# Performance work log

Hardware: AMD Instinct MI355X
Metric: run time of the kernel (lower is better)

The kernel has to match this reference:

```python
import jax, jax.numpy as jnp
import numpy as np

N = 100000   # nodes
E = 1000000  # edges (before self-loops)
IN = 128     # in_channel
HID = 32     # hidden_channels
H1 = 8       # in_head
OUT = 40     # out_channel
NEG_SLOPE = 0.2


def setup_inputs() -> dict:
    key = jax.random.key(0)
    ks = jax.random.split(key, 12)
    s = 0.05
    return {
        "x0": jax.random.normal(ks[0], (N, IN), jnp.float32),
        "W1": jax.random.normal(ks[1], (IN, H1 * HID), jnp.float32) * s,
        "att_src1": jax.random.normal(ks[2], (H1, HID), jnp.float32) * s,
        "att_dst1": jax.random.normal(ks[3], (H1, HID), jnp.float32) * s,
        "b1": jnp.zeros((H1 * HID,), jnp.float32),
        "W2": jax.random.normal(ks[4], (H1 * HID, 1 * HID), jnp.float32) * s,
        "att_src2": jax.random.normal(ks[5], (1, HID), jnp.float32) * s,
        "att_dst2": jax.random.normal(ks[6], (1, HID), jnp.float32) * s,
        "b2": jnp.zeros((HID,), jnp.float32),
        "linW": jax.random.normal(ks[7], (HID, OUT), jnp.float32) * s,
        "linb": jnp.zeros((OUT,), jnp.float32),
        "edge_index": jax.random.randint(ks[8], (2, E), 0, N, dtype=jnp.int64),
    }


def gat_conv(x, src, dst, W, att_src, att_dst, bias, concat):
    # PyG GATConv (eval mode): per-head linear, edge attention, dst-softmax, scatter-add
    H, C = att_src.shape
    h = (x @ W).reshape(N, H, C)                       # [N,H,C]
    a_src = jnp.sum(h * att_src[None], axis=-1)        # [N,H]
    a_dst = jnp.sum(h * att_dst[None], axis=-1)        # [N,H]
    alpha = jax.nn.leaky_relu(a_src[src] + a_dst[dst], NEG_SLOPE)  # [Etot,H]
    m = jax.ops.segment_max(alpha, dst, num_segments=N)           # [N,H]
    ea = jnp.exp(alpha - m[dst])
    denom = jax.ops.segment_sum(ea, dst, num_segments=N)
    w = ea / jnp.clip(denom, 1e-16, None)[dst]          # [Etot,H]
    out = jax.ops.segment_sum(w[:, :, None] * h[src], dst, num_segments=N)  # [N,H,C]
    out = out.reshape(N, H * C) if concat else jnp.mean(out, axis=1)
    return out + bias


def reference(x0, W1, att_src1, att_dst1, b1, W2, att_src2, att_dst2, b2, linW, linb, edge_index):
    # add self-loops (PyG add_self_loops=True default)
    loop = jnp.arange(N, dtype=edge_index.dtype)
    src = jnp.concatenate([edge_index[0], loop])
    dst = jnp.concatenate([edge_index[1], loop])
    # dropout layers are no-ops in eval mode
    x1 = gat_conv(x0, src, dst, W1, att_src1, att_dst1, b1, concat=True)   # [N, 8*HID]
    x2 = jax.nn.relu(x1)
    x2 = gat_conv(x2, src, dst, W2, att_src2, att_dst2, b2, concat=False)  # [N, HID]
    return x2 @ linW + linb                                                 # [N, OUT]
```

## Files before the change

### kernel.cpp

```cpp
#include <hip/hip_runtime.h>

#define N 100000
#define E 1000000
#define ETOT 1100000
#define NB1 391
#define NBE 4297
#define NBH (NBE * 8)
#define NBG 782
#define BUCKET 12500

typedef __attribute__((ext_vector_type(8))) short bf16x8;
typedef __attribute__((ext_vector_type(4))) float f32x4;
typedef __attribute__((ext_vector_type(2))) float f32x2;

__device__ __forceinline__ float lrelu(float x) { return x > 0.f ? x : 0.2f * x; }
__device__ __forceinline__ unsigned short f2b(float x) {
    unsigned u = __float_as_uint(x);
    return (unsigned short)((u + 0x7FFFu + ((u >> 16) & 1u)) >> 16);
}
__device__ __forceinline__ float b2f(unsigned short v) {
    return __uint_as_float(((unsigned)v) << 16);
}
__device__ __forceinline__ unsigned char f2q(float x) {
    return (unsigned char)(__builtin_amdgcn_cvt_pk_fp8_f32(x, x, 0, false) & 0xFF);
}

__global__ __launch_bounds__(256) void prep_kernel(const int* __restrict__ ei,
                                                   int* __restrict__ hist,
                                                   const float* __restrict__ W1,
                                                   const float* __restrict__ W2,
                                                   const float* __restrict__ att_src1,
                                                   const float* __restrict__ att_dst1,
                                                   unsigned short* __restrict__ W1T,
                                                   unsigned short* __restrict__ W2T) {
    const int b = blockIdx.x;
    const int t = threadIdx.x;
    if (b < NBH) {
        const int w = b >> 3;
        const int k = b & 7;
        const int e = w * 256 + t;
        if (e < ETOT) {
            int d = (e < E) ? ei[E + e] : (e - E);
            if (d / BUCKET == k) atomicAdd(&hist[d], 1);
        }
        return;
    }
    const int bb = b - NBH;
    if (bb < 128) {
        W1T[(size_t)t * 128 + bb] = f2b(W1[(size_t)bb * 256 + t]);
    } else if (bb < 160) {
        int n = bb - 128;
        W2T[(size_t)n * 256 + t] = f2b(W2[(size_t)t * 32 + n]);
    } else {
        int idx = (bb - 160) * 256 + t;
        int col = idx >> 7;
        int k = idx & 127;
        int h = col & 7;
        const float* att = (col < 8) ? att_src1 : att_dst1;
        float acc = 0.f;
#pragma unroll 8
        for (int j = 0; j < 32; j++) acc += W1[(size_t)k * 256 + h * 32 + j] * att[h * 32 + j];
        W1T[(size_t)(256 + col) * 128 + k] = f2b(acc);
    }
}

__global__ __launch_bounds__(256) void g1s_kernel(const float* __restrict__ x0,
                                                  const unsigned short* __restrict__ W1T,
                                                  unsigned char* __restrict__ h1,
                                                  float* __restrict__ a_src,
                                                  float* __restrict__ a_dst,
                                                  const int* __restrict__ hist,
                                                  int* __restrict__ rofs,
                                                  int* __restrict__ bsum) {
    __shared__ int sm[256];
    if (blockIdx.x >= NBG) {
        const int blk = blockIdx.x - NBG;
        const int t = threadIdx.x;
        const int i = blk * 256 + t;
        int v = (i < N) ? hist[i] : 0;
        sm[t] = v;
        __syncthreads();
#pragma unroll
        for (int off = 1; off < 256; off <<= 1) {
            int x = (t >= off) ? sm[t - off] : 0;
            __syncthreads();
            sm[t] += x;
            __syncthreads();
        }
        if (i < N) rofs[i] = sm[t] - v;
        if (t == 255) bsum[blk] = sm[255];
        return;
    }
    const int wv = threadIdx.x >> 6;
    const int lane = threadIdx.x & 63;
    const int quad = lane >> 4, c = lane & 15;
    const int base_m = blockIdx.x * 128 + wv * 32;
    const int l = c & 3;
    const unsigned sel1 = (l & 1) ? 0x07030501u : 0x02060004u;
    const unsigned sel2 = (l & 2) ? 0x07060302u : 0x01000504u;
    bf16x8 af[2][4];
#pragma unroll
    for (int mt = 0; mt < 2; mt++) {
        int row = base_m + mt * 16 + c;
        int rowc = row < N ? row : N - 1;
        const float* ap = x0 + (size_t)rowc * 128 + quad * 8;
#pragma unroll
        for (int ks = 0; ks < 4; ks++) {
            float4 lo = *(const float4*)(ap + ks * 32);
            float4 hi = *(const float4*)(ap + ks * 32 + 4);
            bf16x8 f;
            f[0] = (short)f2b(lo.x); f[1] = (short)f2b(lo.y);
            f[2] = (short)f2b(lo.z); f[3] = (short)f2b(lo.w);
            f[4] = (short)f2b(hi.x); f[5] = (short)f2b(hi.y);
            f[6] = (short)f2b(hi.z); f[7] = (short)f2b(hi.w);
            af[mt][ks] = f;
        }
    }
    for (int nt = 0; nt < 17; nt++) {
        f32x4 acc0 = {0.f, 0.f, 0.f, 0.f};
        f32x4 acc1 = {0.f, 0.f, 0.f, 0.f};
#pragma unroll
        for (int ks = 0; ks < 4; ks++) {
            bf16x8 bf = *(const bf16x8*)(W1T + (size_t)(nt * 16 + c) * 128 + ks * 32 + quad * 8);
            acc0 = __builtin_amdgcn_mfma_f32_16x16x32_bf16(af[0][ks], bf, acc0, 0, 0, 0);
            acc1 = __builtin_amdgcn_mfma_f32_16x16x32_bf16(af[1][ks], bf, acc1, 0, 0, 0);
        }
        if (nt < 16) {
            const int colb = nt * 16 + (c & 12);
            unsigned w0 = __builtin_amdgcn_cvt_pk_fp8_f32(acc0[0], acc0[1], 0u, false);
            w0 = __builtin_amdgcn_cvt_pk_fp8_f32(acc0[2], acc0[3], w0, true);
            unsigned w1 = __builtin_amdgcn_cvt_pk_fp8_f32(acc1[0], acc1[1], 0u, false);
            w1 = __builtin_amdgcn_cvt_pk_fp8_f32(acc1[2], acc1[3], w1, true);
            unsigned p0 = (unsigned)__shfl_xor((int)w0, 1, 64);
            unsigned p1 = (unsigned)__shfl_xor((int)w1, 1, 64);
            unsigned x0t = __builtin_amdgcn_perm(w0, p0, sel1);
            unsigned x1t = __builtin_amdgcn_perm(w1, p1, sel1);
            unsigned q0 = (unsigned)__shfl_xor((int)x0t, 2, 64);
            unsigned q1 = (unsigned)__shfl_xor((int)x1t, 2, 64);
            unsigned t0 = __builtin_amdgcn_perm(x0t, q0, sel2);
            unsigned t1 = __builtin_amdgcn_perm(x1t, q1, sel2);
            int r0 = base_m + quad * 4 + l;
            if (r0 < N) *(unsigned*)(h1 + (size_t)r0 * 256 + colb) = t0;
            int r1 = base_m + 16 + quad * 4 + l;
            if (r1 < N) *(unsigned*)(h1 + (size_t)r1 * 256 + colb) = t1;
        } else {
            float* dst = (c < 8) ? a_src : a_dst;
            int hh = c & 7;
#pragma unroll
            for (int r = 0; r < 4; r++) {
                int row0 = base_m + quad * 4 + r;
                if (row0 < N) dst[(size_t)row0 * 8 + hh] = acc0[r];
                int row1 = base_m + 16 + quad * 4 + r;
                if (row1 < N) dst[(size_t)row1 * 8 + hh] = acc1[r];
            }
        }
    }
}

__global__ __launch_bounds__(256) void scan23_kernel(int* __restrict__ rofs,
                                                     const int* __restrict__ bsum,
                                                     int* __restrict__ cursor) {
    __shared__ int red[4];
    const int blk = blockIdx.x;
    const int t = threadIdx.x;
    int v = 0;
    for (int j = t; j < blk; j += 256) v += bsum[j];
#pragma unroll
    for (int off = 1; off < 64; off <<= 1) v += __shfl_xor(v, off, 64);
    if ((t & 63) == 0) red[t >> 6] = v;
    __syncthreads();
    const int prefix = (red[0] + red[1]) + (red[2] + red[3]);
    const int i = blk * 256 + t;
    if (i < N) {
        int r = rofs[i] + prefix;
        rofs[i] = r;
        cursor[i] = r;
    }
    if (i == 0) rofs[N] = ETOT;
}

__global__ __launch_bounds__(256) void scatter_kernel(const int* __restrict__ ei,
                                                      int* __restrict__ cursor,
                                                      int* __restrict__ esrc) {
    const int w = blockIdx.x >> 3;
    const int k = blockIdx.x & 7;
    const int e = w * 256 + threadIdx.x;
    if (e >= ETOT) return;
    int s, d;
    if (e < E) { s = ei[e]; d = ei[E + e]; } else { s = d = e - E; }
    if (d / BUCKET != k) return;
    int pos = atomicAdd(&cursor[d], 1);
    esrc[pos] = s;
}

__global__ __launch_bounds__(256) void seg1_kernel(const int* __restrict__ esrc,
                                                   const int* __restrict__ rofs,
                                                   const float* __restrict__ a_src,
                                                   const float* __restrict__ a_dst,
                                                   const unsigned char* __restrict__ h1,
                                                   const float* __restrict__ b1,
                                                   unsigned short* __restrict__ x2) {
    const int n = (blockIdx.x * 256 + threadIdx.x) >> 6;
    const int lane = threadIdx.x & 63;
    const int e_pa = lane >> 3;
    const int h_pa = lane & 7;
    const int hB = lane >> 3;
    const int rs = __builtin_amdgcn_readfirstlane(rofs[n]);
    const int re = __builtin_amdgcn_readfirstlane(rofs[n + 1]);
    const float ad_pa = a_dst[(size_t)n * 8 + h_pa];
    float dsum = 0.f;
    float4 Aa = {0, 0, 0, 0}, Ab = {0, 0, 0, 0};
    for (int j0 = rs; j0 < re; j0 += 8) {
        int jm = j0 + e_pa;
        int jc = jm < re ? jm : re - 1;
        int s8 = esrc[jc];
        float av = a_src[(size_t)s8 * 8 + h_pa];
        float ex = __expf(lrelu(av + ad_pa));
        float w = (jm < re) ? ex : 0.f;
        dsum += w;
#pragma unroll
        for (int e = 0; e < 8; e++) {
            float wb = __shfl(w, e * 8 + hB, 64);
            int se = __builtin_amdgcn_readlane(s8, e * 8);
            unsigned hv = ((const unsigned*)(h1 + (size_t)se * 256))[lane];
            f32x2 lo = __builtin_amdgcn_cvt_pk_f32_fp8(hv, false);
            f32x2 hi = __builtin_amdgcn_cvt_pk_f32_fp8(hv, true);
            if (e & 1) {
                Ab.x += wb * lo[0]; Ab.y += wb * lo[1];
                Ab.z += wb * hi[0]; Ab.w += wb * hi[1];
            } else {
                Aa.x += wb * lo[0]; Aa.y += wb * lo[1];
                Aa.z += wb * hi[0]; Aa.w += wb * hi[1];
            }
        }
    }
    dsum += __shfl_xor(dsum, 8, 64);
    dsum += __shfl_xor(dsum, 16, 64);
    dsum += __shfl_xor(dsum, 32, 64);
    float den = __shfl(dsum, hB, 64);
    float4 acc = {Aa.x + Ab.x, Aa.y + Ab.y, Aa.z + Ab.z, Aa.w + Ab.w};
    const float inv = 1.0f / den;
    float4 bb = ((const float4*)b1)[lane];
    float vx = acc.x * inv + bb.x, vy = acc.y * inv + bb.y;
    float vz = acc.z * inv + bb.z, vw = acc.w * inv + bb.w;
    vx = vx > 0.f ? vx : 0.f; vy = vy > 0.f ? vy : 0.f;
    vz = vz > 0.f ? vz : 0.f; vw = vw > 0.f ? vw : 0.f;
    ushort4 o = {f2b(vx), f2b(vy), f2b(vz), f2b(vw)};
    ((ushort4*)(x2 + (size_t)n * 256))[lane] = o;
}

__global__ __launch_bounds__(256) void gemm2_kernel(const unsigned short* __restrict__ x2,
                                                    const unsigned short* __restrict__ W2T,
                                                    const float* __restrict__ att_src2,
                                                    const float* __restrict__ att_dst2,
                                                    unsigned short* __restrict__ h2,
                                                    float* __restrict__ a_src2,
                                                    float* __restrict__ a_dst2) {
    const int wv = threadIdx.x >> 6;
    const int lane = threadIdx.x & 63;
    const int quad = lane >> 4, c = lane & 15;
    const int base_m = blockIdx.x * 128 + wv * 32;
    f32x4 acc[2][2] = {{{0, 0, 0, 0}, {0, 0, 0, 0}}, {{0, 0, 0, 0}, {0, 0, 0, 0}}};
#pragma unroll
    for (int ks = 0; ks < 8; ks++) {
        bf16x8 b0 = *(const bf16x8*)(W2T + (size_t)c * 256 + ks * 32 + quad * 8);
        bf16x8 b1 = *(const bf16x8*)(W2T + (size_t)(16 + c) * 256 + ks * 32 + quad * 8);
#pragma unroll
        for (int mt = 0; mt < 2; mt++) {
            int row = base_m + mt * 16 + c;
            int rowc = row < N ? row : N - 1;
            bf16x8 a = *(const bf16x8*)(x2 + (size_t)rowc * 256 + ks * 32 + quad * 8);
            acc[mt][0] = __builtin_amdgcn_mfma_f32_16x16x32_bf16(a, b0, acc[mt][0], 0, 0, 0);
            acc[mt][1] = __builtin_amdgcn_mfma_f32_16x16x32_bf16(a, b1, acc[mt][1], 0, 0, 0);
        }
    }
    float as0 = att_src2[c], as1 = att_src2[16 + c];
    float ad0 = att_dst2[c], ad1 = att_dst2[16 + c];
#pragma unroll
    for (int mt = 0; mt < 2; mt++) {
#pragma unroll
        for (int r = 0; r < 4; r++) {
            int row = base_m + mt * 16 + quad * 4 + r;
            float v0 = acc[mt][0][r], v1 = acc[mt][1][r];
            float ps = v0 * as0 + v1 * as1;
            float pd = v0 * ad0 + v1 * ad1;
#pragma unroll
            for (int off = 1; off < 16; off <<= 1) {
                ps += __shfl_xor(ps, off, 64);
                pd += __shfl_xor(pd, off, 64);
            }
            if (row < N) {
                h2[(size_t)row * 32 + c] = f2b(v0);
                h2[(size_t)row * 32 + 16 + c] = f2b(v1);
                if (c == 0) { a_src2[row] = ps; a_dst2[row] = pd; }
            }
        }
    }
}

__global__ __launch_bounds__(256) void seg2_kernel(const int* __restrict__ esrc,
                                                   const int* __restrict__ rofs,
                                                   const float* __restrict__ a_src2,
                                                   const float* __restrict__ a_dst2,
                                                   const unsigned short* __restrict__ h2,
                                                   const float* __restrict__ b2,
                                                   const float* __restrict__ linW,
                                                   const float* __restrict__ linb,
                                                   float* __restrict__ out) {
    __shared__ float lws[32 * 41];
    __shared__ float vbuf[8][33];
    const int t = threadIdx.x;
    for (int i = t; i < 1280; i += 256) {
        int ci = i / 40, o = i - ci * 40;
        lws[ci * 41 + o] = linW[i];
    }
    const int n8 = t >> 5;
    const int c = t & 31;
    const int myk = t & 7;
    const int n = blockIdx.x * 8 + n8;
    const int rs = rofs[n], re = rofs[n + 1];
    const float ad = a_dst2[n];
    float dsum = 0.f;
    float A[8] = {0, 0, 0, 0, 0, 0, 0, 0};
    for (int j0 = rs; j0 < re; j0 += 8) {
        int sidx[8];
#pragma unroll
        for (int k = 0; k < 8; k++) {
            int j = j0 + k;
            sidx[k] = esrc[j < re ? j : re - 1];
        }
        float av = a_src2[sidx[myk]];
        float myw = (j0 + myk < re) ? __expf(lrelu(av + ad)) : 0.f;
        dsum += myw;
        unsigned short hb[8];
#pragma unroll
        for (int k = 0; k < 8; k++) hb[k] = h2[(size_t)sidx[k] * 32 + c];
#pragma unroll
        for (int k = 0; k < 8; k++) {
            float w = __shfl(myw, (t & 32) + k, 64);
            A[k] += w * b2f(hb[k]);
        }
    }
    dsum += __shfl_xor(dsum, 1, 64);
    dsum += __shfl_xor(dsum, 2, 64);
    dsum += __shfl_xor(dsum, 4, 64);
    float acc = ((A[0] + A[1]) + (A[2] + A[3])) + ((A[4] + A[5]) + (A[6] + A[7]));
    vbuf[n8][c] = acc / dsum + b2[c];
    __syncthreads();
    for (int idx = t; idx < 320; idx += 256) {
        int nn = idx / 40, o = idx - nn * 40;
        float s = linb[o];
#pragma unroll
        for (int ci = 0; ci < 32; ci++) s += vbuf[nn][ci] * lws[ci * 41 + o];
        out[(size_t)blockIdx.x * 320 + idx] = s;
    }
}

extern "C" void kernel_launch(void* const* d_in, const int* in_sizes, int n_in,
                              void* d_out, int out_size, void* d_ws, size_t ws_size,
                              hipStream_t stream) {
    const float* x0       = (const float*)d_in[0];
    const float* W1       = (const float*)d_in[1];
    const float* att_src1 = (const float*)d_in[2];
    const float* att_dst1 = (const float*)d_in[3];
    const float* b1       = (const float*)d_in[4];
    const float* W2       = (const float*)d_in[5];
    const float* att_src2 = (const float*)d_in[6];
    const float* att_dst2 = (const float*)d_in[7];
    const float* b2       = (const float*)d_in[8];
    const float* linW     = (const float*)d_in[9];
    const float* linb     = (const float*)d_in[10];
    const int*   ei       = (const int*)d_in[11];
    float* out = (float*)d_out;
    float* ws  = (float*)d_ws;

    unsigned char* h1    = (unsigned char*)ws;
    unsigned short* x2   = (unsigned short*)(ws + 6400000);
    float* a_src1        = ws + 19200000;
    float* a_dst1        = ws + 20000000;
    unsigned short* h2   = (unsigned short*)(ws + 20800000);
    float* a_src2        = ws + 22400000;
    float* a_dst2        = ws + 22500000;
    unsigned short* W1T  = (unsigned short*)(ws + 22600000);
    unsigned short* W2T  = (unsigned short*)(ws + 22620000);
    int*   hist          = (int*)(ws + 22630000);
    int*   rofs          = (int*)(ws + 22730000);
    int*   cursor        = (int*)(ws + 22840000);
    int*   bsum          = (int*)(ws + 22940000);
    int*   esrc          = (int*)(ws + 22941000);

    hipMemsetAsync(hist, 0, (size_t)N * 4, stream);

    prep_kernel<<<NBH + 168, 256, 0, stream>>>(ei, hist, W1, W2, att_src1, att_dst1, W1T, W2T);
    g1s_kernel<<<NBG + NB1, 256, 0, stream>>>(x0, W1T, h1, a_src1, a_dst1, hist, rofs, bsum);
    scan23_kernel<<<NB1, 256, 0, stream>>>(rofs, bsum, cursor);
    scatter_kernel<<<NBE * 8, 256, 0, stream>>>(ei, cursor, esrc);

    seg1_kernel<<<N / 4, 256, 0, stream>>>(esrc, rofs, a_src1, a_dst1, h1, b1, x2);
    gemm2_kernel<<<(N + 127) / 128, 256, 0, stream>>>(x2, W2T, att_src2, att_dst2, h2, a_src2, a_dst2);
    seg2_kernel<<<N / 8, 256, 0, stream>>>(esrc, rofs, a_src2, a_dst2, h2, b2, linW, linb, out);
}
```

Measured before the change: 360.8 us.

## Fuse layer-1 aggregation with layer-2 GEMM and grid-stride histogram/scatter

Merges the layer-1 segment aggregation and the layer-2 MFMA GEMM into one kernel. Each 1024-thread block aggregates 16 nodes into shared memory, then one wave multiplies that 16x256 tile by W2, so the bf16 x2 intermediate never goes through global memory. The histogram and scatter kernels change from one block per edge chunk per bucket to a fixed 2048-block grid-stride loop, which cuts the block count. The trade-offs are a block-wide barrier with only one wave doing the GEMM, W2T reloaded by every block, and a different atomic ordering pattern.

```diff
diff --git a/kernel.cpp b/kernel.cpp
--- a/kernel.cpp
+++ b/kernel.cpp
@@ -5,7 +5,7 @@
 #define ETOT 1100000
 #define NB1 391
 #define NBE 4297
-#define NBH (NBE * 8)
+#define NPREP 2048
 #define NBG 782
 #define BUCKET 12500
 
@@ -35,17 +35,18 @@
                                                    unsigned short* __restrict__ W2T) {
     const int b = blockIdx.x;
     const int t = threadIdx.x;
-    if (b < NBH) {
-        const int w = b >> 3;
+    if (b < NPREP) {
         const int k = b & 7;
-        const int e = w * 256 + t;
-        if (e < ETOT) {
-            int d = (e < E) ? ei[E + e] : (e - E);
-            if (d / BUCKET == k) atomicAdd(&hist[d], 1);
+        for (int w = b >> 3; w < NBE; w += 256) {
+            const int e = w * 256 + t;
+            if (e < ETOT) {
+                int d = (e < E) ? ei[E + e] : (e - E);
+                if (d / BUCKET == k) atomicAdd(&hist[d], 1);
+            }
         }
         return;
     }
-    const int bb = b - NBH;
+    const int bb = b - NPREP;
     if (bb < 128) {
         W1T[(size_t)t * 128 + bb] = f2b(W1[(size_t)bb * 256 + t]);
     } else if (bb < 160) {
@@ -182,26 +183,34 @@
 __global__ __launch_bounds__(256) void scatter_kernel(const int* __restrict__ ei,
                                                       int* __restrict__ cursor,
                                                       int* __restrict__ esrc) {
-    const int w = blockIdx.x >> 3;
     const int k = blockIdx.x & 7;
-    const int e = w * 256 + threadIdx.x;
-    if (e >= ETOT) return;
-    int s, d;
-    if (e < E) { s = ei[e]; d = ei[E + e]; } else { s = d = e - E; }
-    if (d / BUCKET != k) return;
-    int pos = atomicAdd(&cursor[d], 1);
-    esrc[pos] = s;
-}
-
-__global__ __launch_bounds__(256) void seg1_kernel(const int* __restrict__ esrc,
-                                                   const int* __restrict__ rofs,
-                                                   const float* __restrict__ a_src,
-                                                   const float* __restrict__ a_dst,
-                                                   const unsigned char* __restrict__ h1,
-                                                   const float* __restrict__ b1,
-                                                   unsigned short* __restrict__ x2) {
-    const int n = (blockIdx.x * 256 + threadIdx.x) >> 6;
+    for (int w = blockIdx.x >> 3; w < NBE; w += 256) {
+        const int e = w * 256 + threadIdx.x;
+        if (e >= ETOT) continue;
+        int s, d;
+        if (e < E) { s = ei[e]; d = ei[E + e]; } else { s = d = e - E; }
+        if (d / BUCKET != k) continue;
+        int pos = atomicAdd(&cursor[d], 1);
+        esrc[pos] = s;
+    }
+}
+
+__global__ __launch_bounds__(1024, 8) void s1g2_kernel(const int* __restrict__ esrc,
+                                                       const int* __restrict__ rofs,
+                                                       const float* __restrict__ a_src,
+                                                       const float* __restrict__ a_dst,
+                                                       const unsigned char* __restrict__ h1,
+                                                       const float* __restrict__ b1,
+                                                       const unsigned short* __restrict__ W2T,
+                                                       const float* __restrict__ att_src2,
+                                                       const float* __restrict__ att_dst2,
+                                                       unsigned short* __restrict__ h2,
+                                                       float* __restrict__ a_src2,
+                                                       float* __restrict__ a_dst2) {
+    __shared__ unsigned short smx[16 * 264];
+    const int wv = threadIdx.x >> 6;
     const int lane = threadIdx.x & 63;
+    const int n = blockIdx.x * 16 + wv;
     const int e_pa = lane >> 3;
     const int h_pa = lane & 7;
     const int hB = lane >> 3;
@@ -246,42 +255,26 @@
     vx = vx > 0.f ? vx : 0.f; vy = vy > 0.f ? vy : 0.f;
     vz = vz > 0.f ? vz : 0.f; vw = vw > 0.f ? vw : 0.f;
     ushort4 o = {f2b(vx), f2b(vy), f2b(vz), f2b(vw)};
-    ((ushort4*)(x2 + (size_t)n * 256))[lane] = o;
-}
-
-__global__ __launch_bounds__(256) void gemm2_kernel(const unsigned short* __restrict__ x2,
-                                                    const unsigned short* __restrict__ W2T,
-                                                    const float* __restrict__ att_src2,
-                                                    const float* __restrict__ att_dst2,
-                                                    unsigned short* __restrict__ h2,
-                                                    float* __restrict__ a_src2,
-                                                    float* __restrict__ a_dst2) {
-    const int wv = threadIdx.x >> 6;
-    const int lane = threadIdx.x & 63;
-    const int quad = lane >> 4, c = lane & 15;
-    const int base_m = blockIdx.x * 128 + wv * 32;
-    f32x4 acc[2][2] = {{{0, 0, 0, 0}, {0, 0, 0, 0}}, {{0, 0, 0, 0}, {0, 0, 0, 0}}};
-#pragma unroll
-    for (int ks = 0; ks < 8; ks++) {
-        bf16x8 b0 = *(const bf16x8*)(W2T + (size_t)c * 256 + ks * 32 + quad * 8);
-        bf16x8 b1 = *(const bf16x8*)(W2T + (size_t)(16 + c) * 256 + ks * 32 + quad * 8);
-#pragma unroll
-        for (int mt = 0; mt < 2; mt++) {
-            int row = base_m + mt * 16 + c;
-            int rowc = row < N ? row : N - 1;
-            bf16x8 a = *(const bf16x8*)(x2 + (size_t)rowc * 256 + ks * 32 + quad * 8);
-            acc[mt][0] = __builtin_amdgcn_mfma_f32_16x16x32_bf16(a, b0, acc[mt][0], 0, 0, 0);
-            acc[mt][1] = __builtin_amdgcn_mfma_f32_16x16x32_bf16(a, b1, acc[mt][1], 0, 0, 0);
-        }
-    }
-    float as0 = att_src2[c], as1 = att_src2[16 + c];
-    float ad0 = att_dst2[c], ad1 = att_dst2[16 + c];
-#pragma unroll
-    for (int mt = 0; mt < 2; mt++) {
+    *(ushort4*)(smx + wv * 264 + lane * 4) = o;
+    __syncthreads();
+    if (threadIdx.x < 64) {
+        const int quad = lane >> 4, c = lane & 15;
+        const int base_m = blockIdx.x * 16;
+        f32x4 g[2] = {{0, 0, 0, 0}, {0, 0, 0, 0}};
+#pragma unroll
+        for (int ks = 0; ks < 8; ks++) {
+            bf16x8 a = *(const bf16x8*)(smx + c * 264 + ks * 32 + quad * 8);
+            bf16x8 b0 = *(const bf16x8*)(W2T + (size_t)c * 256 + ks * 32 + quad * 8);
+            bf16x8 b1v = *(const bf16x8*)(W2T + (size_t)(16 + c) * 256 + ks * 32 + quad * 8);
+            g[0] = __builtin_amdgcn_mfma_f32_16x16x32_bf16(a, b0, g[0], 0, 0, 0);
+            g[1] = __builtin_amdgcn_mfma_f32_16x16x32_bf16(a, b1v, g[1], 0, 0, 0);
+        }
+        float as0 = att_src2[c], as1 = att_src2[16 + c];
+        float ad0 = att_dst2[c], ad1 = att_dst2[16 + c];
 #pragma unroll
         for (int r = 0; r < 4; r++) {
-            int row = base_m + mt * 16 + quad * 4 + r;
-            float v0 = acc[mt][0][r], v1 = acc[mt][1][r];
+            int row = base_m + quad * 4 + r;
+            float v0 = g[0][r], v1 = g[1][r];
             float ps = v0 * as0 + v1 * as1;
             float pd = v0 * ad0 + v1 * ad1;
 #pragma unroll
@@ -289,11 +282,9 @@
                 ps += __shfl_xor(ps, off, 64);
                 pd += __shfl_xor(pd, off, 64);
             }
-            if (row < N) {
-                h2[(size_t)row * 32 + c] = f2b(v0);
-                h2[(size_t)row * 32 + 16 + c] = f2b(v1);
-                if (c == 0) { a_src2[row] = ps; a_dst2[row] = pd; }
-            }
+            h2[(size_t)row * 32 + c] = f2b(v0);
+            h2[(size_t)row * 32 + 16 + c] = f2b(v1);
+            if (c == 0) { a_src2[row] = ps; a_dst2[row] = pd; }
         }
     }
 }
@@ -375,7 +366,6 @@
     float* ws  = (float*)d_ws;
 
     unsigned char* h1    = (unsigned char*)ws;
-    unsigned short* x2   = (unsigned short*)(ws + 6400000);
     float* a_src1        = ws + 19200000;
     float* a_dst1        = ws + 20000000;
     unsigned short* h2   = (unsigned short*)(ws + 20800000);
@@ -391,12 +381,11 @@
 
     hipMemsetAsync(hist, 0, (size_t)N * 4, stream);
 
-    prep_kernel<<<NBH + 168, 256, 0, stream>>>(ei, hist, W1, W2, att_src1, att_dst1, W1T, W2T);
+    prep_kernel<<<NPREP + 168, 256, 0, stream>>>(ei, hist, W1, W2, att_src1, att_dst1, W1T, W2T);
     g1s_kernel<<<NBG + NB1, 256, 0, stream>>>(x0, W1T, h1, a_src1, a_dst1, hist, rofs, bsum);
     scan23_kernel<<<NB1, 256, 0, stream>>>(rofs, bsum, cursor);
-    scatter_kernel<<<NBE * 8, 256, 0, stream>>>(ei, cursor, esrc);
-
-    seg1_kernel<<<N / 4, 256, 0, stream>>>(esrc, rofs, a_src1, a_dst1, h1, b1, x2);
-    gemm2_kernel<<<(N + 127) / 128, 256, 0, stream>>>(x2, W2T, att_src2, att_dst2, h2, a_src2, a_dst2);
+    scatter_kernel<<<NPREP, 256, 0, stream>>>(ei, cursor, esrc);
+    s1g2_kernel<<<N / 16, 1024, 0, stream>>>(esrc, rofs, a_src1, a_dst1, h1, b1,
+                                             W2T, att_src2, att_dst2, h2, a_src2, a_dst2);
     seg2_kernel<<<N / 8, 256, 0, stream>>>(esrc, rofs, a_src2, a_dst2, h2, b2, linW, linb, out);
 }
```

Measured after the change: 358.9 us. No clear change (-0.5%).
